# Performance work log

Measured on AMD Instinct MI355X. Metric: run time of the kernel, lower is better.

The kernel has to match this reference:

```python
import jax, jax.numpy as jnp
import numpy as np

B, C, N, K = 4, 64, 8192, 16
OUT = 128

def setup_inputs() -> dict:
    key = jax.random.key(0)
    k1, k2, k3, k4 = jax.random.split(key, 4)
    x = jax.random.normal(k1, (B, C, N, 1), dtype=jnp.float32)
    edge_index = jax.random.randint(k2, (2, B, N, K), 0, N)
    # BasicConv([2C, OUT]) is a 1x1 Conv2d -> weight [OUT, 2C], bias [OUT]
    W_nn = jax.random.normal(k3, (OUT, 2 * C), dtype=jnp.float32) * 0.02
    b_nn = jax.random.normal(k4, (OUT,), dtype=jnp.float32) * 0.02
    return {"x": x, "edge_index": edge_index, "W_nn": W_nn, "b_nn": b_nn}

def _gather_nodes(x2, idx):
    # x2: [B, C, N], idx: [B, N, K] -> [B, C, N, K]
    return jax.vmap(lambda xb, ib: xb[:, ib])(x2, idx)

def reference(x, edge_index, W_nn, b_nn):
    b, c, n, _ = x.shape
    x2 = x[:, :, :, 0]                      # [B, C, N]
    x_i = _gather_nodes(x2, edge_index[1])  # [B, C, N, K]
    x_j = _gather_nodes(x2, edge_index[0])  # [B, C, N, K]
    x_j = jnp.max(x_j - x_i, axis=-1, keepdims=True)  # [B, C, N, 1]
    # interleave channels: cat([x.unsqueeze(2), x_j.unsqueeze(2)], dim=2).reshape(b, 2c, n, 1)
    h = jnp.concatenate([x[:, :, None], x_j[:, :, None]], axis=2).reshape(b, 2 * c, n, 1)
    # BasicConv: 1x1 conv + bias + ReLU
    out = jnp.einsum('oc,bcn->bon', W_nn, h[:, :, :, 0]) + b_nn[None, :, None]
    return jax.nn.relu(out)[:, :, :, None]  # [B, OUT, N, 1]
```

## Files before the change

### kernel.cpp

```cpp
#include <hip/hip_runtime.h>
#include <cstddef>

#define BB 4
#define CC 64
#define NN 8192
#define KK 16
#define OO 128

#define SH 136

typedef __attribute__((ext_vector_type(8))) short bf16x8;
typedef __attribute__((ext_vector_type(4))) float f32x4;

__device__ __forceinline__ unsigned short f2b(float f) {
    unsigned u = __builtin_bit_cast(unsigned, f);
    unsigned r = (u + 0x7fffu + ((u >> 16) & 1u)) >> 16;
    return (unsigned short)r;
}

__device__ __forceinline__ float bclo(unsigned d) {
    return __builtin_bit_cast(float, d << 16);
}
__device__ __forceinline__ float bchi(unsigned d) {
    return __builtin_bit_cast(float, d & 0xffff0000u);
}

__global__ __launch_bounds__(256) void transpose_kernel(
        const float* __restrict__ x, unsigned short* __restrict__ xt,
        const float* __restrict__ W, unsigned short* __restrict__ Wbf) {
    __shared__ float tile[64][65];
    const int b  = blockIdx.y;
    const int n0 = blockIdx.x * 64;
    const int t  = threadIdx.x;
    const int ln = t & 63;
    const int r  = t >> 6;

    const float* xb = x + (size_t)b * CC * NN;
    #pragma unroll
    for (int s = 0; s < 64; s += 4) {
        int c = s + r;
        tile[c][ln] = xb[(size_t)c * NN + n0 + ln];
    }
    __syncthreads();
    unsigned short* xtb = xt + ((size_t)b * NN + n0) * CC;
    #pragma unroll
    for (int s = 0; s < 64; s += 4) {
        int n = s + r;
        xtb[n * CC + ln] = f2b(tile[ln][n]);
    }

    if (b == 0 && blockIdx.x < 16) {
        int idx = blockIdx.x * 1024 + t * 4;
        float4 v = *reinterpret_cast<const float4*>(W + idx);
        ushort4 o;
        o.x = f2b(v.x); o.y = f2b(v.y); o.z = f2b(v.z); o.w = f2b(v.w);
        *reinterpret_cast<ushort4*>(Wbf + idx) = o;
    }
}

__global__ __launch_bounds__(256, 4) void main_kernel(
        const unsigned short* __restrict__ xt,
        const unsigned short* __restrict__ Wbf,
        const int*            __restrict__ eidx,
        const float*          __restrict__ bias,
        float*                __restrict__ out) {
    __shared__ unsigned short hl[64 * SH];
    __shared__ int eL[2048];

    const int t    = threadIdx.x;
    const int lane = t & 63;
    const int w    = t >> 6;
    const int b    = blockIdx.y;
    const int n_base = blockIdx.x * 64;

    const int* e0 = eidx + ((size_t)b * NN + n_base) * KK;
    const int* e1 = e0 + (size_t)BB * NN * KK;
    *reinterpret_cast<int4*>(&eL[t * 4])        = *reinterpret_cast<const int4*>(e0 + t * 4);
    *reinterpret_cast<int4*>(&eL[1024 + t * 4]) = *reinterpret_cast<const int4*>(e1 + t * 4);

    const int quad = lane >> 4;
    const int l15  = lane & 15;
    const int o0w  = w * 32;
    bf16x8 afr[2][4];
    #pragma unroll
    for (int ot = 0; ot < 2; ot++)
        #pragma unroll
        for (int ks = 0; ks < 4; ks++)
            afr[ot][ks] = *reinterpret_cast<const bf16x8*>(
                Wbf + (o0w + ot * 16 + l15) * OO + ks * 32 + quad * 8);

    __syncthreads();

    const unsigned short* xtb = xt + (size_t)b * NN * CC;
    const int g = lane >> 3;
    const int p = lane & 7;

    #pragma unroll
    for (int bt = 0; bt < 2; bt++) {
        const int nl = w * 16 + bt * 8 + g;
        uint4 xr = *reinterpret_cast<const uint4*>(xtb + (size_t)(n_base + nl) * CC + p * 8);

        float m[8];
        #pragma unroll
        for (int j = 0; j < 8; j++) m[j] = -1e30f;

        #pragma unroll
        for (int q = 0; q < 4; q++) {
            int kj[4], ki[4];
            #pragma unroll
            for (int k4 = 0; k4 < 4; k4++) {
                int k = q * 4 + k4;
                kj[k4] = eL[nl * KK + k];
                ki[k4] = eL[1024 + nl * KK + k];
            }
            uint4 aj[4], ai[4];
            #pragma unroll
            for (int k4 = 0; k4 < 4; k4++)
                aj[k4] = *reinterpret_cast<const uint4*>(xtb + (size_t)kj[k4] * CC + p * 8);
            #pragma unroll
            for (int k4 = 0; k4 < 4; k4++)
                ai[k4] = *reinterpret_cast<const uint4*>(xtb + (size_t)ki[k4] * CC + p * 8);
            #pragma unroll
            for (int k4 = 0; k4 < 4; k4++) {
                m[0] = fmaxf(m[0], bclo(aj[k4].x) - bclo(ai[k4].x));
                m[1] = fmaxf(m[1], bchi(aj[k4].x) - bchi(ai[k4].x));
                m[2] = fmaxf(m[2], bclo(aj[k4].y) - bclo(ai[k4].y));
                m[3] = fmaxf(m[3], bchi(aj[k4].y) - bchi(ai[k4].y));
                m[4] = fmaxf(m[4], bclo(aj[k4].z) - bclo(ai[k4].z));
                m[5] = fmaxf(m[5], bchi(aj[k4].z) - bchi(ai[k4].z));
                m[6] = fmaxf(m[6], bclo(aj[k4].w) - bclo(ai[k4].w));
                m[7] = fmaxf(m[7], bchi(aj[k4].w) - bchi(ai[k4].w));
            }
        }

        unsigned xs[8];
        xs[0] = xr.x & 0xffffu; xs[1] = xr.x >> 16;
        xs[2] = xr.y & 0xffffu; xs[3] = xr.y >> 16;
        xs[4] = xr.z & 0xffffu; xs[5] = xr.z >> 16;
        xs[6] = xr.w & 0xffffu; xs[7] = xr.w >> 16;
        uint4 lo, hi;
        lo.x = xs[0] | ((unsigned)f2b(m[0]) << 16);
        lo.y = xs[1] | ((unsigned)f2b(m[1]) << 16);
        lo.z = xs[2] | ((unsigned)f2b(m[2]) << 16);
        lo.w = xs[3] | ((unsigned)f2b(m[3]) << 16);
        hi.x = xs[4] | ((unsigned)f2b(m[4]) << 16);
        hi.y = xs[5] | ((unsigned)f2b(m[5]) << 16);
        hi.z = xs[6] | ((unsigned)f2b(m[6]) << 16);
        hi.w = xs[7] | ((unsigned)f2b(m[7]) << 16);
        unsigned short* dst = &hl[nl * SH + p * 16];
        *reinterpret_cast<uint4*>(dst)     = lo;
        *reinterpret_cast<uint4*>(dst + 8) = hi;
    }
    __syncthreads();

    #pragma unroll
    for (int nt = 0; nt < 4; nt++) {
        f32x4 acc0 = {0.f, 0.f, 0.f, 0.f};
        f32x4 acc1 = {0.f, 0.f, 0.f, 0.f};
        #pragma unroll
        for (int ks = 0; ks < 4; ks++) {
            const unsigned short* bp = &hl[(nt * 16 + l15) * SH + ks * 32 + quad * 8];
            bf16x8 bfr = *reinterpret_cast<const bf16x8*>(bp);
            acc0 = __builtin_amdgcn_mfma_f32_16x16x32_bf16(afr[0][ks], bfr, acc0, 0, 0, 0);
            acc1 = __builtin_amdgcn_mfma_f32_16x16x32_bf16(afr[1][ks], bfr, acc1, 0, 0, 0);
        }
        int n_g = n_base + nt * 16 + l15;
        #pragma unroll
        for (int r = 0; r < 4; r++) {
            int o_a = o0w + quad * 4 + r;
            int o_b = o0w + 16 + quad * 4 + r;
            float va = acc0[r] + bias[o_a];
            float vb = acc1[r] + bias[o_b];
            out[((size_t)b * OO + o_a) * NN + n_g] = fmaxf(va, 0.f);
            out[((size_t)b * OO + o_b) * NN + n_g] = fmaxf(vb, 0.f);
        }
    }
}

extern "C" void kernel_launch(void* const* d_in, const int* in_sizes, int n_in,
                              void* d_out, int out_size, void* d_ws, size_t ws_size,
                              hipStream_t stream) {
    const float* x    = (const float*)d_in[0];
    const int*   eidx = (const int*)d_in[1];
    const float* W    = (const float*)d_in[2];
    const float* bias = (const float*)d_in[3];
    float* out = (float*)d_out;

    unsigned short* xt  = (unsigned short*)d_ws;
    unsigned short* Wbf = (unsigned short*)((char*)d_ws + 4 * 1024 * 1024);

    dim3 blk(256);
    dim3 grid(NN / 64, BB);
    transpose_kernel<<<grid, blk, 0, stream>>>(x, xt, W, Wbf);
    main_kernel<<<grid, blk, 0, stream>>>(xt, Wbf, eidx, bias, out);
}
```

Measured before the change: 83.61 us.

## Interleave two nodes per gather round and remap blocks across batches

```diff
diff --git a/kernel.cpp b/kernel.cpp
--- a/kernel.cpp
+++ b/kernel.cpp
@@ -25,12 +25,18 @@
     return __builtin_bit_cast(float, d & 0xffff0000u);
 }
 
+__device__ __forceinline__ void decode_block(int i, int& b, int& n_base) {
+    b = i & 3;
+    int nblk = ((i >> 2) & 1) * 64 + (i >> 3);
+    n_base = nblk * 64;
+}
+
 __global__ __launch_bounds__(256) void transpose_kernel(
         const float* __restrict__ x, unsigned short* __restrict__ xt,
         const float* __restrict__ W, unsigned short* __restrict__ Wbf) {
     __shared__ float tile[64][65];
-    const int b  = blockIdx.y;
-    const int n0 = blockIdx.x * 64;
+    int b, n0;
+    decode_block(blockIdx.x, b, n0);
     const int t  = threadIdx.x;
     const int ln = t & 63;
     const int r  = t >> 6;
@@ -49,7 +55,7 @@
         xtb[n * CC + ln] = f2b(tile[ln][n]);
     }
 
-    if (b == 0 && blockIdx.x < 16) {
+    if (blockIdx.x < 16) {
         int idx = blockIdx.x * 1024 + t * 4;
         float4 v = *reinterpret_cast<const float4*>(W + idx);
         ushort4 o;
@@ -70,13 +76,96 @@
     const int t    = threadIdx.x;
     const int lane = t & 63;
     const int w    = t >> 6;
-    const int b    = blockIdx.y;
-    const int n_base = blockIdx.x * 64;
+    int b, n_base;
+    decode_block(blockIdx.x, b, n_base);
 
     const int* e0 = eidx + ((size_t)b * NN + n_base) * KK;
     const int* e1 = e0 + (size_t)BB * NN * KK;
     *reinterpret_cast<int4*>(&eL[t * 4])        = *reinterpret_cast<const int4*>(e0 + t * 4);
     *reinterpret_cast<int4*>(&eL[1024 + t * 4]) = *reinterpret_cast<const int4*>(e1 + t * 4);
+    __syncthreads();
+
+    const unsigned short* xtb = xt + (size_t)b * NN * CC;
+    const int g = lane >> 3;
+    const int p = lane & 7;
+    const int nl0 = w * 16 + g;
+    const int nl1 = nl0 + 8;
+
+    uint4 xr0 = *reinterpret_cast<const uint4*>(xtb + (size_t)(n_base + nl0) * CC + p * 8);
+    uint4 xr1 = *reinterpret_cast<const uint4*>(xtb + (size_t)(n_base + nl1) * CC + p * 8);
+
+    float m0[8], m1[8];
+    #pragma unroll
+    for (int j = 0; j < 8; j++) { m0[j] = -1e30f; m1[j] = -1e30f; }
+
+    for (int q = 0; q < 4; q++) {
+        int4 kj0 = *reinterpret_cast<const int4*>(&eL[nl0 * KK + q * 4]);
+        int4 ki0 = *reinterpret_cast<const int4*>(&eL[1024 + nl0 * KK + q * 4]);
+        int4 kj1 = *reinterpret_cast<const int4*>(&eL[nl1 * KK + q * 4]);
+        int4 ki1 = *reinterpret_cast<const int4*>(&eL[1024 + nl1 * KK + q * 4]);
+        int ja[8] = {kj0.x, kj0.y, kj0.z, kj0.w, kj1.x, kj1.y, kj1.z, kj1.w};
+        int ia[8] = {ki0.x, ki0.y, ki0.z, ki0.w, ki1.x, ki1.y, ki1.z, ki1.w};
+
+        uint4 aj[8], ai[8];
+        #pragma unroll
+        for (int u = 0; u < 8; u++)
+            aj[u] = *reinterpret_cast<const uint4*>(xtb + (size_t)ja[u] * CC + p * 8);
+        #pragma unroll
+        for (int u = 0; u < 8; u++)
+            ai[u] = *reinterpret_cast<const uint4*>(xtb + (size_t)ia[u] * CC + p * 8);
+
+        #pragma unroll
+        for (int u = 0; u < 8; u++) {
+            float* m = (u < 4) ? m0 : m1;
+            m[0] = fmaxf(m[0], bclo(aj[u].x) - bclo(ai[u].x));
+            m[1] = fmaxf(m[1], bchi(aj[u].x) - bchi(ai[u].x));
+            m[2] = fmaxf(m[2], bclo(aj[u].y) - bclo(ai[u].y));
+            m[3] = fmaxf(m[3], bchi(aj[u].y) - bchi(ai[u].y));
+            m[4] = fmaxf(m[4], bclo(aj[u].z) - bclo(ai[u].z));
+            m[5] = fmaxf(m[5], bchi(aj[u].z) - bchi(ai[u].z));
+            m[6] = fmaxf(m[6], bclo(aj[u].w) - bclo(ai[u].w));
+            m[7] = fmaxf(m[7], bchi(aj[u].w) - bchi(ai[u].w));
+        }
+    }
+
+    {
+        unsigned xs[8];
+        xs[0] = xr0.x & 0xffffu; xs[1] = xr0.x >> 16;
+        xs[2] = xr0.y & 0xffffu; xs[3] = xr0.y >> 16;
+        xs[4] = xr0.z & 0xffffu; xs[5] = xr0.z >> 16;
+        xs[6] = xr0.w & 0xffffu; xs[7] = xr0.w >> 16;
+        uint4 lo, hi;
+        lo.x = xs[0] | ((unsigned)f2b(m0[0]) << 16);
+        lo.y = xs[1] | ((unsigned)f2b(m0[1]) << 16);
+        lo.z = xs[2] | ((unsigned)f2b(m0[2]) << 16);
+        lo.w = xs[3] | ((unsigned)f2b(m0[3]) << 16);
+        hi.x = xs[4] | ((unsigned)f2b(m0[4]) << 16);
+        hi.y = xs[5] | ((unsigned)f2b(m0[5]) << 16);
+        hi.z = xs[6] | ((unsigned)f2b(m0[6]) << 16);
+        hi.w = xs[7] | ((unsigned)f2b(m0[7]) << 16);
+        unsigned short* dst = &hl[nl0 * SH + p * 16];
+        *reinterpret_cast<uint4*>(dst)     = lo;
+        *reinterpret_cast<uint4*>(dst + 8) = hi;
+    }
+    {
+        unsigned xs[8];
+        xs[0] = xr1.x & 0xffffu; xs[1] = xr1.x >> 16;
+        xs[2] = xr1.y & 0xffffu; xs[3] = xr1.y >> 16;
+        xs[4] = xr1.z & 0xffffu; xs[5] = xr1.z >> 16;
+        xs[6] = xr1.w & 0xffffu; xs[7] = xr1.w >> 16;
+        uint4 lo, hi;
+        lo.x = xs[0] | ((unsigned)f2b(m1[0]) << 16);
+        lo.y = xs[1] | ((unsigned)f2b(m1[1]) << 16);
+        lo.z = xs[2] | ((unsigned)f2b(m1[2]) << 16);
+        lo.w = xs[3] | ((unsigned)f2b(m1[3]) << 16);
+        hi.x = xs[4] | ((unsigned)f2b(m1[4]) << 16);
+        hi.y = xs[5] | ((unsigned)f2b(m1[5]) << 16);
+        hi.z = xs[6] | ((unsigned)f2b(m1[6]) << 16);
+        hi.w = xs[7] | ((unsigned)f2b(m1[7]) << 16);
+        unsigned short* dst = &hl[nl1 * SH + p * 16];
+        *reinterpret_cast<uint4*>(dst)     = lo;
+        *reinterpret_cast<uint4*>(dst + 8) = hi;
+    }
 
     const int quad = lane >> 4;
     const int l15  = lane & 15;
@@ -89,68 +178,6 @@
             afr[ot][ks] = *reinterpret_cast<const bf16x8*>(
                 Wbf + (o0w + ot * 16 + l15) * OO + ks * 32 + quad * 8);
 
-    __syncthreads();
-
-    const unsigned short* xtb = xt + (size_t)b * NN * CC;
-    const int g = lane >> 3;
-    const int p = lane & 7;
-
-    #pragma unroll
-    for (int bt = 0; bt < 2; bt++) {
-        const int nl = w * 16 + bt * 8 + g;
-        uint4 xr = *reinterpret_cast<const uint4*>(xtb + (size_t)(n_base + nl) * CC + p * 8);
-
-        float m[8];
-        #pragma unroll
-        for (int j = 0; j < 8; j++) m[j] = -1e30f;
-
-        #pragma unroll
-        for (int q = 0; q < 4; q++) {
-            int kj[4], ki[4];
-            #pragma unroll
-            for (int k4 = 0; k4 < 4; k4++) {
-                int k = q * 4 + k4;
-                kj[k4] = eL[nl * KK + k];
-                ki[k4] = eL[1024 + nl * KK + k];
-            }
-            uint4 aj[4], ai[4];
-            #pragma unroll
-            for (int k4 = 0; k4 < 4; k4++)
-                aj[k4] = *reinterpret_cast<const uint4*>(xtb + (size_t)kj[k4] * CC + p * 8);
-            #pragma unroll
-            for (int k4 = 0; k4 < 4; k4++)
-                ai[k4] = *reinterpret_cast<const uint4*>(xtb + (size_t)ki[k4] * CC + p * 8);
-            #pragma unroll
-            for (int k4 = 0; k4 < 4; k4++) {
-                m[0] = fmaxf(m[0], bclo(aj[k4].x) - bclo(ai[k4].x));
-                m[1] = fmaxf(m[1], bchi(aj[k4].x) - bchi(ai[k4].x));
-                m[2] = fmaxf(m[2], bclo(aj[k4].y) - bclo(ai[k4].y));
-                m[3] = fmaxf(m[3], bchi(aj[k4].y) - bchi(ai[k4].y));
-                m[4] = fmaxf(m[4], bclo(aj[k4].z) - bclo(ai[k4].z));
-                m[5] = fmaxf(m[5], bchi(aj[k4].z) - bchi(ai[k4].z));
-                m[6] = fmaxf(m[6], bclo(aj[k4].w) - bclo(ai[k4].w));
-                m[7] = fmaxf(m[7], bchi(aj[k4].w) - bchi(ai[k4].w));
-            }
-        }
-
-        unsigned xs[8];
-        xs[0] = xr.x & 0xffffu; xs[1] = xr.x >> 16;
-        xs[2] = xr.y & 0xffffu; xs[3] = xr.y >> 16;
-        xs[4] = xr.z & 0xffffu; xs[5] = xr.z >> 16;
-        xs[6] = xr.w & 0xffffu; xs[7] = xr.w >> 16;
-        uint4 lo, hi;
-        lo.x = xs[0] | ((unsigned)f2b(m[0]) << 16);
-        lo.y = xs[1] | ((unsigned)f2b(m[1]) << 16);
-        lo.z = xs[2] | ((unsigned)f2b(m[2]) << 16);
-        lo.w = xs[3] | ((unsigned)f2b(m[3]) << 16);
-        hi.x = xs[4] | ((unsigned)f2b(m[4]) << 16);
-        hi.y = xs[5] | ((unsigned)f2b(m[5]) << 16);
-        hi.z = xs[6] | ((unsigned)f2b(m[6]) << 16);
-        hi.w = xs[7] | ((unsigned)f2b(m[7]) << 16);
-        unsigned short* dst = &hl[nl * SH + p * 16];
-        *reinterpret_cast<uint4*>(dst)     = lo;
-        *reinterpret_cast<uint4*>(dst + 8) = hi;
-    }
     __syncthreads();
 
     #pragma unroll
@@ -190,7 +217,7 @@
     unsigned short* Wbf = (unsigned short*)((char*)d_ws + 4 * 1024 * 1024);
 
     dim3 blk(256);
-    dim3 grid(NN / 64, BB);
+    dim3 grid(512);
     transpose_kernel<<<grid, blk, 0, stream>>>(x, xt, W, Wbf);
     main_kernel<<<grid, blk, 0, stream>>>(xt, Wbf, eidx, bias, out);
 }
```

Result: no change. 83.79 us (+0.2%).
